# Kernel tuning notes

Measured on AMD Instinct MI355X. Metric: run time of the kernel, lower is better.

Reference implementation:

```python
import jax, jax.numpy as jnp
import numpy as np

# ---- static lookup-point config (matches cfg.radius/stride/level) ----
RADIUS = [4, 4, 4, 4]
STRIDE = [1, 1, 1, 1]
LEVEL = [0, 1, 2, 3]

def _build_pts():
    pts = {}
    for r, s, l in zip(RADIUS, STRIDE, LEVEL):
        pts.setdefault(l, set())
        for x in range(-r, r + 1):
            for y in range(-r, r + 1):
                pts[l].add((x * s, y * s))
    # sorted() reproduces torch's `v.sort()` on (x, y) tuples
    return {l: np.array(sorted(v), dtype=np.float32) for l, v in sorted(pts.items())}

PTS = _build_pts()                       # {lvl: (n_lvl, 2) offsets in level pixels}
N_LEVELS = max(LEVEL) + 1                # 4
CORR_DIM = 2 * sum(len(v) for v in PTS.values())   # 648
C_HALF = CORR_DIM // 2                   # 324 = per-direction channels
B, C, H, W = 1, 256, 80, 80


def _bilinear_sample(corr, x, y):
    """corr: (B, P, h, w); x, y: (P, n) pixel coords (align_corners=False convention,
    already converted to pixel space). Zero padding outside. Returns (B, P, n)."""
    Bn, P, h, w = corr.shape
    cf = corr.reshape(Bn, P, h * w)
    x0 = jnp.floor(x)
    y0 = jnp.floor(y)
    wx1 = x - x0
    wy1 = y - y0
    x0i = x0.astype(jnp.int32)
    y0i = y0.astype(jnp.int32)
    out = jnp.zeros((Bn, P, x.shape[-1]), corr.dtype)
    for dx, wxx in ((0, 1.0 - wx1), (1, wx1)):
        for dy, wyy in ((0, 1.0 - wy1), (1, wy1)):
            xi = x0i + dx
            yi = y0i + dy
            valid = (xi >= 0) & (xi < w) & (yi >= 0) & (yi < h)
            idx = jnp.clip(yi, 0, h - 1) * w + jnp.clip(xi, 0, w - 1)   # (P, n)
            v = jnp.take_along_axis(cf, jnp.broadcast_to(idx[None], (Bn,) + idx.shape), axis=2)
            out = out + v * (wxx * wyy * valid)[None]
    return out


def _lookup_pyramid(pyr):
    """pyr[lvl]: (B, P, H>>lvl, W>>lvl). Returns (B, P, C_HALF)."""
    outs = []
    for lvl, pts in PTS.items():
        s = 1 << lvl
        n = pts.shape[0]
        dxy = jnp.asarray(pts)
        # grid_sample align_corners=False: level-pixel coord of full-res pixel j is
        # (2j+1)/(2s) - 0.5; neighbor offsets are exactly `pts` in level pixels.
        bx = (2.0 * jnp.arange(W) + 1.0) / (2.0 * s) - 0.5   # (W,)
        by = (2.0 * jnp.arange(H) + 1.0) / (2.0 * s) - 0.5   # (H,)
        x = jnp.broadcast_to(bx[None, :, None] + dxy[None, None, :, 0], (H, W, n)).reshape(H * W, n)
        y = jnp.broadcast_to(by[:, None, None] + dxy[None, None, :, 1], (H, W, n)).reshape(H * W, n)
        outs.append(_bilinear_sample(pyr[lvl], x, y))
    return jnp.concatenate(outs, axis=-1)


def _pyramid(corr):
    """corr: (B, P, H, W) -> list of avg-pooled levels (2x2, stride 2)."""
    p = [corr]
    for _ in range(N_LEVELS - 1):
        b, pp, h, w = corr.shape
        corr = corr.reshape(b, pp, h // 2, 2, w // 2, 2).mean(axis=(3, 5))
        p.append(corr)
    return p


def _conv3x3_relu(x, w, b):
    y = jax.lax.conv_general_dilated(x, w, (1, 1), 'SAME',
                                     dimension_numbers=('NHWC', 'HWIO', 'NHWC'))
    return jax.nn.relu(y + b)


def _layer_norm(x, g, b, eps=1e-5):
    m = x.mean(-1, keepdims=True)
    v = ((x - m) ** 2).mean(-1, keepdims=True)
    return (x - m) * jax.lax.rsqrt(v + eps) * g + b


def setup_inputs() -> dict:
    key = jax.random.key(0)
    ks = jax.random.split(key, 4)
    return {
        'f0': jax.random.normal(ks[0], (B, C, H, W), jnp.float32),
        'f1': jax.random.normal(ks[1], (B, C, H, W), jnp.float32),
        'conv_w1': jax.random.normal(ks[2], (3, 3, C_HALF, C_HALF), jnp.float32) * 0.02,
        'conv_b1': jnp.zeros((C_HALF,), jnp.float32),
        'conv_w2': jax.random.normal(ks[3], (3, 3, C_HALF, C_HALF), jnp.float32) * 0.02,
        'conv_b2': jnp.zeros((C_HALF,), jnp.float32),
        'ln_g': jnp.ones((C_HALF,), jnp.float32),
        'ln_b': jnp.zeros((C_HALF,), jnp.float32),
    }


def reference(f0, f1, conv_w1, conv_b1, conv_w2, conv_b2, ln_g, ln_b):
    Bn, Cn, Hn, Wn = f0.shape
    P = Hn * Wn
    a = f0.reshape(Bn, Cn, P)
    bb = f1.reshape(Bn, Cn, P)
    corr01 = jnp.einsum('bcp,bcq->bpq', a, bb)          # (B, P, P)
    corr10 = jnp.swapaxes(corr01, 1, 2)
    feat01 = _lookup_pyramid(_pyramid(corr01.reshape(Bn, P, Hn, Wn)))   # (B, P, C_HALF)
    feat10 = _lookup_pyramid(_pyramid(corr10.reshape(Bn, P, Hn, Wn)))

    def branch(feat):
        x = feat.reshape(Bn, Hn, Wn, C_HALF)
        y = x + _conv3x3_relu(_conv3x3_relu(x, conv_w1, conv_b1), conv_w2, conv_b2)
        y = _layer_norm(y, ln_g, ln_b)
        return jnp.transpose(y, (0, 3, 1, 2))           # (B, C_HALF, H, W)

    return jnp.concatenate([branch(feat01), branch(feat10)], axis=1)    # (B, 2*C_HALF, H, W)
```

## Files before the change

kernel.cpp:

```cpp
#include <hip/hip_runtime.h>

typedef unsigned short u16;
typedef unsigned int   u32;
typedef float f32x4 __attribute__((ext_vector_type(4)));
typedef __bf16 bf16x8 __attribute__((ext_vector_type(8)));
typedef unsigned short u16x8 __attribute__((ext_vector_type(8)));

#define PP   6400
#define HH   80
#define WW   80
#define KC   256
#define CH   324
#define CPAD 384
#define PW   82
#define PPIX (PW*PW)
#define NPOOL 2176

__device__ inline float b2f(u16 u) { union { u32 i; float f; } v; v.i = ((u32)u) << 16; return v.f; }
__device__ inline u16 f2b(float f) {
    union { u32 i; float f; } v; v.f = f;
    u32 r = v.i + 0x7fffu + ((v.i >> 16) & 1u);
    return (u16)(r >> 16);
}

__device__ __forceinline__ void gload16(const void* g, void* l) {
    __builtin_amdgcn_global_load_lds((const __attribute__((address_space(1))) void*)g,
                                     (__attribute__((address_space(3))) void*)l, 16, 0, 0);
}

__global__ __launch_bounds__(256) void prep_f(const float* __restrict__ f0,
                                              const float* __restrict__ f1,
                                              u16* __restrict__ fA, u16* __restrict__ fB) {
    __shared__ float tile[64][65];
    int p0 = blockIdx.x * 64, c0 = blockIdx.y * 64;
    const float* src = blockIdx.z ? f1 : f0;
    u16* dst = blockIdx.z ? fB : fA;
    int tid = threadIdx.x;
#pragma unroll
    for (int it = 0; it < 16; ++it) {
        int idx = tid + it * 256;
        int cc = idx >> 6, pp = idx & 63;
        tile[cc][pp] = src[(size_t)(c0 + cc) * PP + p0 + pp];
    }
    __syncthreads();
#pragma unroll
    for (int it = 0; it < 16; ++it) {
        int idx = tid + it * 256;
        int pp = idx >> 6, cc = idx & 63;
        dst[(size_t)(p0 + pp) * KC + c0 + cc] = f2b(tile[cc][pp]);
    }
}

__global__ __launch_bounds__(256) void prep_w(const float* __restrict__ w1,
                                              const float* __restrict__ w2,
                                              u16* __restrict__ wT1, u16* __restrict__ wT2) {
    __shared__ float tile[64][65];
    int tap = blockIdx.x;
    int t6 = blockIdx.y;
    int ci0 = (t6 / 6) * 64, co0 = (t6 % 6) * 64;
    const float* w = blockIdx.z ? w2 : w1;
    u16* wT = blockIdx.z ? wT2 : wT1;
    int tid = threadIdx.x;
#pragma unroll
    for (int it = 0; it < 16; ++it) {
        int idx = tid + it * 256;
        int ciL = idx >> 6, coL = idx & 63;
        int ci = ci0 + ciL, co = co0 + coL;
        tile[ciL][coL] = (ci < CH && co < CH) ? w[((size_t)tap * CH + ci) * CH + co] : 0.f;
    }
    __syncthreads();
#pragma unroll
    for (int it = 0; it < 16; ++it) {
        int idx = tid + it * 256;
        int coL = idx >> 6, ciL = idx & 63;
        wT[((size_t)tap * CPAD + co0 + coL) * CPAD + ci0 + ciL] = f2b(tile[ciL][coL]);
    }
}

__global__ __launch_bounds__(384) void zero_border(u16* __restrict__ feat, u16* __restrict__ t1,
                                                   const float* __restrict__ b1,
                                                   const float* __restrict__ b2,
                                                   float* __restrict__ b1p, float* __restrict__ b2p) {
    int bi = blockIdx.x, dir = blockIdx.y;
    int t = threadIdx.x;
    if (bi == 324) {
        if (dir == 0) b1p[t] = t < CH ? b1[t] : 0.f;
        else          b2p[t] = t < CH ? b2[t] : 0.f;
        return;
    }
    int pix;
    if (bi < 82) pix = bi;
    else if (bi < 164) pix = 81 * PW + (bi - 82);
    else if (bi < 244) pix = (bi - 164 + 1) * PW;
    else pix = (bi - 244 + 1) * PW + 81;
    size_t off = ((size_t)dir * PPIX + pix) * CPAD + t;
    feat[off] = 0;
    t1[off] = 0;
}

__global__ __launch_bounds__(256) void pool_feat(const u16* __restrict__ fA,
                                                 const u16* __restrict__ fB,
                                                 u16* __restrict__ pbarA,
                                                 u16* __restrict__ pbarB) {
    int j = blockIdx.x;
    const u16* src = blockIdx.y ? fA : fB;
    u16* dst = blockIdx.y ? pbarA : pbarB;
    int k = threadIdx.x;
    int cy3 = j / 10, cx3 = j % 10;
    float l1v[16], l2v[4];
#pragma unroll
    for (int a = 0; a < 4; ++a)
#pragma unroll
        for (int b = 0; b < 4; ++b) {
            int cy = cy3 * 4 + a, cx = cx3 * 4 + b;
            int p00 = (2 * cy) * 80 + 2 * cx;
            float v = 0.25f * (b2f(src[(size_t)p00 * KC + k]) + b2f(src[(size_t)(p00 + 1) * KC + k]) +
                               b2f(src[(size_t)(p00 + 80) * KC + k]) + b2f(src[(size_t)(p00 + 81) * KC + k]));
            l1v[a * 4 + b] = v;
            dst[(size_t)(cy * 40 + cx) * KC + k] = f2b(v);
        }
#pragma unroll
    for (int a = 0; a < 2; ++a)
#pragma unroll
        for (int b = 0; b < 2; ++b) {
            float v = 0.25f * (l1v[(2 * a) * 4 + 2 * b] + l1v[(2 * a) * 4 + 2 * b + 1] +
                               l1v[(2 * a + 1) * 4 + 2 * b] + l1v[(2 * a + 1) * 4 + 2 * b + 1]);
            l2v[a * 2 + b] = v;
            dst[(size_t)(1600 + (cy3 * 2 + a) * 20 + cx3 * 2 + b) * KC + k] = f2b(v);
        }
    float v3 = 0.25f * (l2v[0] + l2v[1] + l2v[2] + l2v[3]);
    dst[(size_t)(2000 + j) * KC + k] = f2b(v3);
}

__global__ __launch_bounds__(256) void gemm_cp(const u16* __restrict__ fA,
                                               const u16* __restrict__ fB,
                                               const u16* __restrict__ pbarA,
                                               const u16* __restrict__ pbarB,
                                               u16* __restrict__ corr01,
                                               u16* __restrict__ corr10,
                                               u16* __restrict__ pc) {
    int y = blockIdx.y, z = blockIdx.z;
    bool band = (y < 7);
    int m0 = blockIdx.x * 128, n0;
    const u16 *Aptr, *Bptr;
    if (band) {
        if (z) return;
        int n0t = (int)blockIdx.x + y - 3;
        if (n0t < 0 || n0t >= 50) return;
        n0 = n0t * 128;
        Aptr = fA; Bptr = fB;
    } else {
        n0 = (y - 7) * 128;
        Aptr = z ? fB : fA;
        Bptr = z ? pbarA : pbarB;
    }
    __shared__ __align__(16) char smem[128 * 136 * 2];
    u16* As = (u16*)smem;
    u16* Bs = As + 128 * 64;
    u16* trans = (u16*)smem;
    const int TS = 136;
    int tid = threadIdx.x;
    int wave = tid >> 6, lane = tid & 63;
    int quad = lane >> 4, l16 = lane & 15;
    int lrow = lane >> 3, lchunk = lane & 7;
    int sc = lchunk ^ (lrow & 7);
    int sw = l16 & 7;
    int wr = (wave >> 1) * 64, wc = (wave & 1) * 64;
    f32x4 acc[4][4] = {};

    for (int k0 = 0; k0 < KC; k0 += 64) {
        __syncthreads();
#pragma unroll
        for (int i = 0; i < 4; ++i) {
            int row = i * 32 + wave * 8 + lrow;
            gload16(&Aptr[(size_t)(m0 + row) * KC + k0 + sc * 8], &As[(i * 32 + wave * 8) * 64]);
            gload16(&Bptr[(size_t)(n0 + row) * KC + k0 + sc * 8], &Bs[(i * 32 + wave * 8) * 64]);
        }
        __syncthreads();
#pragma unroll
        for (int ki = 0; ki < 2; ++ki) {
            bf16x8 af[4], bfr[4];
#pragma unroll
            for (int mi = 0; mi < 4; ++mi) {
                int r = wr + mi * 16 + l16;
                af[mi] = *(const bf16x8*)(&As[r * 64 + (((ki * 4 + quad) ^ sw) * 8)]);
            }
#pragma unroll
            for (int ni = 0; ni < 4; ++ni) {
                int r = wc + ni * 16 + l16;
                bfr[ni] = *(const bf16x8*)(&Bs[r * 64 + (((ki * 4 + quad) ^ sw) * 8)]);
            }
#pragma unroll
            for (int mi = 0; mi < 4; ++mi)
#pragma unroll
                for (int ni = 0; ni < 4; ++ni)
                    acc[mi][ni] = __builtin_amdgcn_mfma_f32_16x16x32_bf16(af[mi], bfr[ni], acc[mi][ni], 0, 0, 0);
        }
    }
    __syncthreads();
#pragma unroll
    for (int mi = 0; mi < 4; ++mi)
#pragma unroll
        for (int ni = 0; ni < 4; ++ni) {
            int rbase = wr + mi * 16 + quad * 4;
            int c = wc + ni * 16 + l16;
#pragma unroll
            for (int rr = 0; rr < 4; ++rr)
                trans[(rbase + rr) * TS + c] = f2b(acc[mi][ni][rr]);
        }
    __syncthreads();
    if (!band) {
        int dir = z;
#pragma unroll
        for (int it = 0; it < 8; ++it) {
            int r = it * 16 + (tid >> 4);
            int c8 = (tid & 15) * 8;
            u16x8 v = *(const u16x8*)(&trans[r * TS + c8]);
            *(u16x8*)(&pc[((size_t)dir * PP + m0 + r) * NPOOL + n0 + c8]) = v;
        }
        return;
    }
#pragma unroll
    for (int it = 0; it < 8; ++it) {
        int r = it * 16 + (tid >> 4);
        int c8 = (tid & 15) * 8;
        u16x8 v = *(const u16x8*)(&trans[r * TS + c8]);
        *(u16x8*)(&corr01[(size_t)(m0 + r) * PP + n0 + c8]) = v;
    }
    __syncthreads();
#pragma unroll
    for (int mi = 0; mi < 4; ++mi)
#pragma unroll
        for (int ni = 0; ni < 4; ++ni) {
            int c = wc + ni * 16 + l16;
            int rbase = wr + mi * 16 + quad * 4;
#pragma unroll
            for (int h = 0; h < 2; ++h) {
                u32 pk = (u32)f2b(acc[mi][ni][2 * h]) | ((u32)f2b(acc[mi][ni][2 * h + 1]) << 16);
                *(u32*)(&trans[c * TS + rbase + 2 * h]) = pk;
            }
        }
    __syncthreads();
#pragma unroll
    for (int it = 0; it < 8; ++it) {
        int c = it * 16 + (tid >> 4);
        int r8 = (tid & 15) * 8;
        u16x8 v = *(const u16x8*)(&trans[c * TS + r8]);
        *(u16x8*)(&corr10[(size_t)(n0 + c) * PP + m0 + r8]) = v;
    }
}

__global__ __launch_bounds__(384) void lookup(const u16* __restrict__ corr01,
                                              const u16* __restrict__ corr10,
                                              const u16* __restrict__ pc,
                                              u16* __restrict__ feat) {
    __shared__ __align__(16) u16 pcrow[4][NPOOL];
    __shared__ float l0buf[4][81];
    int p0 = blockIdx.x * 4, dir = blockIdx.y;
    int tid = threadIdx.x;
    const u16* corr = dir ? corr10 : corr01;
    for (int i = tid; i < 4 * (NPOOL / 8); i += 384) {
        int j = i / (NPOOL / 8), cc = i % (NPOOL / 8);
        *(u16x8*)(&pcrow[j][cc * 8]) =
            *(const u16x8*)(&pc[((size_t)dir * PP + p0 + j) * NPOOL + cc * 8]);
    }
    if (tid < 324) {
        int j = tid / 81, i = tid % 81;
        int p = p0 + j;
        int px = p % WW, py = p / WW;
        int dy = i / 9 - 4, dx = i % 9 - 4;
        int x = px + dx, yy = py + dy;
        float v = 0.f;
        if ((unsigned)x < (unsigned)WW && (unsigned)yy < (unsigned)HH)
            v = b2f(corr[(size_t)p * PP + yy * WW + x]);
        l0buf[j][(i % 9) * 9 + i / 9] = v;
    }
    __syncthreads();
    int ch = tid;
#pragma unroll
    for (int j = 0; j < 4; ++j) {
        int p = p0 + j;
        int px = p % WW, py = p / WW;
        float val = 0.f;
        if (ch < CH) {
            int lvl = ch / 81, i = ch % 81;
            if (lvl == 0) {
                val = l0buf[j][i];
            } else {
                int dx = i / 9 - 4, dy = i % 9 - 4;
                int wl = WW >> lvl;
                int base = (lvl == 1) ? 0 : (lvl == 2) ? 1600 : 2000;
                float inv = 1.0f / (float)(2 << lvl);
                float xc = (float)(2 * px + 1) * inv - 0.5f + (float)dx;
                float yc = (float)(2 * py + 1) * inv - 0.5f + (float)dy;
                float x0f = floorf(xc), y0f = floorf(yc);
                int x0 = (int)x0f, y0 = (int)y0f;
                float wx = xc - x0f, wy = yc - y0f;
#pragma unroll
                for (int cy = 0; cy < 2; ++cy)
#pragma unroll
                    for (int cx = 0; cx < 2; ++cx) {
                        int xi = x0 + cx, yi = y0 + cy;
                        if ((unsigned)xi < (unsigned)wl && (unsigned)yi < (unsigned)wl) {
                            float wgt = (cx ? wx : 1.f - wx) * (cy ? wy : 1.f - wy);
                            val += b2f(pcrow[j][base + yi * wl + xi]) * wgt;
                        }
                    }
            }
        }
        size_t pix = (size_t)(py + 1) * PW + px + 1;
        feat[((size_t)dir * PPIX + pix) * CPAD + ch] = f2b(val);
    }
}

__global__ __launch_bounds__(256) void conv_gemm(const u16* __restrict__ inFeat,
                                                 const u16* __restrict__ wTt,
                                                 const float* __restrict__ bias,
                                                 const u16* __restrict__ resid,
                                                 u16* __restrict__ outb) {
    int L = (int)blockIdx.x;
    int xcd = L & 7;
    int q = L >> 3;
    int n_t = q % 3; q /= 3;
    int mg = q % 13;
    int dir = q / 13;
    int m_t = mg * 8 + xcd;
    if (m_t >= 100) return;
    const u16* Ain = inFeat + (size_t)dir * PPIX * CPAD;
    const u16* Rin = resid ? resid + (size_t)dir * PPIX * CPAD : (const u16*)0;
    u16* Out = outb + (size_t)dir * PPIX * CPAD;
    __shared__ __align__(16) u16 As[64 * 128];
    __shared__ __align__(16) u16 Bs[128 * 128];
    int tid = threadIdx.x;
    int wave = tid >> 6, lane = tid & 63;
    int quad = lane >> 4, l16 = lane & 15;
    int wr = (wave >> 1) * 32, wc = (wave & 1) * 64;
    int m0 = m_t * 64, n0 = n_t * 128;
    f32x4 acc[2][4] = {};

    int pixA[4], scI[4];
#pragma unroll
    for (int i = 0; i < 4; ++i) {
        int r = wave * 16 + i * 4 + quad;
        int m = m0 + r;
        pixA[i] = (m / 80 + 1) * PW + (m % 80) + 1;
        scI[i] = l16 ^ ((i * 4 + quad) & 15);
    }

    for (int tap = 0; tap < 9; ++tap) {
        int dpix = (tap / 3 - 1) * PW + (tap % 3) - 1;
        const u16* Wt = wTt + ((size_t)tap * CPAD + n0) * CPAD;
#pragma unroll
        for (int kt = 0; kt < 3; ++kt) {
            int kc = kt * 128;
            __syncthreads();
#pragma unroll
            for (int i = 0; i < 4; ++i)
                gload16(&Ain[(size_t)(pixA[i] + dpix) * CPAD + kc + scI[i] * 8],
                        &As[(wave * 16 + i * 4) * 128]);
#pragma unroll
            for (int j = 0; j < 8; ++j) {
                int rb = wave * 32 + j * 4;
                gload16(&Wt[(size_t)(rb + quad) * CPAD + kc + scI[j & 3] * 8],
                        &Bs[rb * 128]);
            }
            __syncthreads();
#pragma unroll
            for (int ki = 0; ki < 4; ++ki) {
                int slot = (ki * 4 + quad) ^ l16;
                bf16x8 af[2], bfr[4];
#pragma unroll
                for (int mi = 0; mi < 2; ++mi)
                    af[mi] = *(const bf16x8*)(&As[(wr + mi * 16 + l16) * 128 + slot * 8]);
#pragma unroll
                for (int ni = 0; ni < 4; ++ni)
                    bfr[ni] = *(const bf16x8*)(&Bs[(wc + ni * 16 + l16) * 128 + slot * 8]);
#pragma unroll
                for (int mi = 0; mi < 2; ++mi)
#pragma unroll
                    for (int ni = 0; ni < 4; ++ni)
                        acc[mi][ni] = __builtin_amdgcn_mfma_f32_16x16x32_bf16(af[mi], bfr[ni], acc[mi][ni], 0, 0, 0);
            }
        }
    }
#pragma unroll
    for (int mi = 0; mi < 2; ++mi)
#pragma unroll
        for (int rr = 0; rr < 4; ++rr) {
            int p = m0 + wr + mi * 16 + quad * 4 + rr;
            size_t opix = (size_t)(p / 80 + 1) * PW + (p % 80) + 1;
#pragma unroll
            for (int ni = 0; ni < 4; ++ni) {
                int co = n0 + wc + ni * 16 + l16;
                float v = acc[mi][ni][rr] + bias[co];
                v = fmaxf(v, 0.f);
                if (Rin) v += b2f(Rin[opix * CPAD + co]);
                Out[opix * CPAD + co] = f2b(v);
            }
        }
}

__global__ __launch_bounds__(256) void ln_out(const u16* __restrict__ t2,
                                              const float* __restrict__ g,
                                              const float* __restrict__ b,
                                              float* __restrict__ out) {
    int dir = blockIdx.y;
    int p0 = blockIdx.x * 64;
    const u16* Y = t2 + (size_t)dir * PPIX * CPAD;
    __shared__ u16 buf[64 * 325];
    __shared__ float mean_s[64], inv_s[64];
    __shared__ float part[64][4][2];
    int tid = threadIdx.x;
    for (int idx = tid; idx < 64 * CH; idx += 256) {
        int pp = idx / CH, c = idx - pp * CH;
        int p = p0 + pp;
        size_t pix = (size_t)(p / 80 + 1) * PW + (p % 80) + 1;
        buf[pp * 325 + c] = Y[pix * CPAD + c];
    }
    __syncthreads();
    {
        int pp = tid >> 2, q = tid & 3;
        float s = 0.f, s2 = 0.f;
        for (int c = q; c < CH; c += 4) { float v = b2f(buf[pp * 325 + c]); s += v; s2 += v * v; }
        part[pp][q][0] = s; part[pp][q][1] = s2;
    }
    __syncthreads();
    if (tid < 64) {
        float s = 0.f, s2 = 0.f;
        for (int q = 0; q < 4; ++q) { s += part[tid][q][0]; s2 += part[tid][q][1]; }
        float m = s / (float)CH;
        float var = s2 / (float)CH - m * m;
        if (var < 0.f) var = 0.f;
        mean_s[tid] = m;
        inv_s[tid] = rsqrtf(var + 1e-5f);
    }
    __syncthreads();
    for (int idx = tid; idx < CH * 64; idx += 256) {
        int c = idx >> 6, pp = idx & 63;
        float v = (b2f(buf[pp * 325 + c]) - mean_s[pp]) * inv_s[pp] * g[c] + b[c];
        out[((size_t)(dir * CH + c)) * PP + p0 + pp] = v;
    }
}

extern "C" void kernel_launch(void* const* d_in, const int* in_sizes, int n_in,
                              void* d_out, int out_size, void* d_ws, size_t ws_size,
                              hipStream_t stream) {
    const float* f0  = (const float*)d_in[0];
    const float* f1  = (const float*)d_in[1];
    const float* w1  = (const float*)d_in[2];
    const float* b1  = (const float*)d_in[3];
    const float* w2  = (const float*)d_in[4];
    const float* b2  = (const float*)d_in[5];
    const float* lng = (const float*)d_in[6];
    const float* lnb = (const float*)d_in[7];
    float* out = (float*)d_out;

    char* ws = (char*)d_ws;
    size_t off = 0;
    auto alloc = [&](size_t bytes) -> char* {
        char* r = ws + off;
        off += (bytes + 511) & ~(size_t)511;
        return r;
    };
    u16* fA     = (u16*)alloc((size_t)PP * KC * 2);
    u16* fB     = (u16*)alloc((size_t)PP * KC * 2);
    u16* corr01 = (u16*)alloc((size_t)PP * PP * 2);
    u16* corr10 = (u16*)alloc((size_t)PP * PP * 2);
    u16* pc     = (u16*)alloc((size_t)2 * PP * NPOOL * 2);
    u16* feat   = (u16*)alloc((size_t)2 * PPIX * CPAD * 2);
    u16* t1     = (u16*)alloc((size_t)2 * PPIX * CPAD * 2);
    u16* t2     = (u16*)alloc((size_t)2 * PPIX * CPAD * 2);
    u16* pbarA  = (u16*)alloc((size_t)NPOOL * KC * 2);
    u16* pbarB  = (u16*)alloc((size_t)NPOOL * KC * 2);
    u16* wT1    = (u16*)alloc((size_t)9 * CPAD * CPAD * 2);
    u16* wT2    = (u16*)alloc((size_t)9 * CPAD * CPAD * 2);
    float* b1p  = (float*)alloc(CPAD * 4);
    float* b2p  = (float*)alloc(CPAD * 4);

    prep_f<<<dim3(100, 4, 2), 256, 0, stream>>>(f0, f1, fA, fB);
    prep_w<<<dim3(9, 36, 2), 256, 0, stream>>>(w1, w2, wT1, wT2);
    zero_border<<<dim3(325, 2), 384, 0, stream>>>(feat, t1, b1, b2, b1p, b2p);
    pool_feat<<<dim3(100, 2), 256, 0, stream>>>(fA, fB, pbarA, pbarB);
    gemm_cp<<<dim3(50, 24, 2), 256, 0, stream>>>(fA, fB, pbarA, pbarB, corr01, corr10, pc);
    lookup<<<dim3(1600, 2), 384, 0, stream>>>(corr01, corr10, pc, feat);
    conv_gemm<<<dim3(624), 256, 0, stream>>>(feat, wT1, b1p, (const u16*)0, t1);
    conv_gemm<<<dim3(624), 256, 0, stream>>>(t1, wT2, b2p, feat, t2);
    ln_out<<<dim3(100, 2), 256, 0, stream>>>(t2, lng, lnb, out);
}
```

Measured before the change: 259.7 us.

## Compute only the pooled-correlation window each row tile actually samples

Pooled correlation columns are now computed only for a window around each 128-row tile. That means 12 rows of level 1, 12 rows of level 2, and all of level 3, instead of all 2176 pooled columns. The pooled GEMM grid shrinks from 17 to 7 column tiles per direction, and the pc buffer and lookup shared memory shrink to 896 columns. The risk is correctness: the window must cover every bilinear tap for every pixel in the tile, and each lookup block must use the same window offsets as the GEMM.

After: 247.5 us. -4.7%, faster.

```diff
diff --git a/kernel.cpp b/kernel.cpp
--- a/kernel.cpp
+++ b/kernel.cpp
@@ -14,7 +14,7 @@
 #define CPAD 384
 #define PW   82
 #define PPIX (PW*PW)
-#define NPOOL 2176
+#define NP2  896
 
 __device__ inline float b2f(u16 u) { union { u32 i; float f; } v; v.i = ((u32)u) << 16; return v.f; }
 __device__ inline u16 f2b(float f) {
@@ -141,7 +141,7 @@
                                                u16* __restrict__ pc) {
     int y = blockIdx.y, z = blockIdx.z;
     bool band = (y < 7);
-    int m0 = blockIdx.x * 128, n0;
+    int m0 = blockIdx.x * 128, n0 = 0, jbase = 0;
     const u16 *Aptr, *Bptr;
     if (band) {
         if (z) return;
@@ -150,10 +150,14 @@
         n0 = n0t * 128;
         Aptr = fA; Bptr = fB;
     } else {
-        n0 = (y - 7) * 128;
+        jbase = (y - 7) * 128;
         Aptr = z ? fB : fA;
         Bptr = z ? pbarA : pbarB;
     }
+    int py0 = m0 / 80;
+    int s1 = min(max(py0 / 2 - 5, 0), 28);
+    int s2 = min(max(py0 / 4 - 5, 0), 8);
+
     __shared__ __align__(16) char smem[128 * 136 * 2];
     u16* As = (u16*)smem;
     u16* Bs = As + 128 * 64;
@@ -168,13 +172,28 @@
     int wr = (wave >> 1) * 64, wc = (wave & 1) * 64;
     f32x4 acc[4][4] = {};
 
+    size_t gRow[4];
+#pragma unroll
+    for (int i = 0; i < 4; ++i) {
+        int row = i * 32 + wave * 8 + lrow;
+        if (band) gRow[i] = (size_t)(n0 + row);
+        else {
+            int j = jbase + row;
+            int g = j < 480 ? s1 * 40 + j
+                  : j < 720 ? 1120 + s2 * 20 + j
+                  : j < 820 ? 1280 + j
+                  : 2099;
+            gRow[i] = (size_t)g;
+        }
+    }
+
     for (int k0 = 0; k0 < KC; k0 += 64) {
         __syncthreads();
 #pragma unroll
         for (int i = 0; i < 4; ++i) {
             int row = i * 32 + wave * 8 + lrow;
             gload16(&Aptr[(size_t)(m0 + row) * KC + k0 + sc * 8], &As[(i * 32 + wave * 8) * 64]);
-            gload16(&Bptr[(size_t)(n0 + row) * KC + k0 + sc * 8], &Bs[(i * 32 + wave * 8) * 64]);
+            gload16(&Bptr[gRow[i] * KC + k0 + sc * 8], &Bs[(i * 32 + wave * 8) * 64]);
         }
         __syncthreads();
 #pragma unroll
@@ -216,7 +235,7 @@
             int r = it * 16 + (tid >> 4);
             int c8 = (tid & 15) * 8;
             u16x8 v = *(const u16x8*)(&trans[r * TS + c8]);
-            *(u16x8*)(&pc[((size_t)dir * PP + m0 + r) * NPOOL + n0 + c8]) = v;
+            *(u16x8*)(&pc[((size_t)dir * PP + m0 + r) * NP2 + jbase + c8]) = v;
         }
         return;
     }
@@ -254,15 +273,19 @@
                                               const u16* __restrict__ corr10,
                                               const u16* __restrict__ pc,
                                               u16* __restrict__ feat) {
-    __shared__ __align__(16) u16 pcrow[4][NPOOL];
+    __shared__ __align__(16) u16 pcrow[4][NP2];
     __shared__ float l0buf[4][81];
     int p0 = blockIdx.x * 4, dir = blockIdx.y;
     int tid = threadIdx.x;
     const u16* corr = dir ? corr10 : corr01;
-    for (int i = tid; i < 4 * (NPOOL / 8); i += 384) {
-        int j = i / (NPOOL / 8), cc = i % (NPOOL / 8);
+    int mt = p0 >> 7;
+    int py0 = (mt * 128) / 80;
+    int s1 = min(max(py0 / 2 - 5, 0), 28);
+    int s2 = min(max(py0 / 4 - 5, 0), 8);
+    for (int i = tid; i < 4 * (NP2 / 8); i += 384) {
+        int j = i / (NP2 / 8), cc = i % (NP2 / 8);
         *(u16x8*)(&pcrow[j][cc * 8]) =
-            *(const u16x8*)(&pc[((size_t)dir * PP + p0 + j) * NPOOL + cc * 8]);
+            *(const u16x8*)(&pc[((size_t)dir * PP + p0 + j) * NP2 + cc * 8]);
     }
     if (tid < 324) {
         int j = tid / 81, i = tid % 81;
@@ -289,7 +312,6 @@
             } else {
                 int dx = i / 9 - 4, dy = i % 9 - 4;
                 int wl = WW >> lvl;
-                int base = (lvl == 1) ? 0 : (lvl == 2) ? 1600 : 2000;
                 float inv = 1.0f / (float)(2 << lvl);
                 float xc = (float)(2 * px + 1) * inv - 0.5f + (float)dx;
                 float yc = (float)(2 * py + 1) * inv - 0.5f + (float)dy;
@@ -303,7 +325,10 @@
                         int xi = x0 + cx, yi = y0 + cy;
                         if ((unsigned)xi < (unsigned)wl && (unsigned)yi < (unsigned)wl) {
                             float wgt = (cx ? wx : 1.f - wx) * (cy ? wy : 1.f - wy);
-                            val += b2f(pcrow[j][base + yi * wl + xi]) * wgt;
+                            int idx = (lvl == 1) ? (yi - s1) * 40 + xi
+                                    : (lvl == 2) ? 480 + (yi - s2) * 20 + xi
+                                                 : 720 + yi * 10 + xi;
+                            val += b2f(pcrow[j][idx]) * wgt;
                         }
                     }
             }
@@ -466,12 +491,12 @@
     u16* fB     = (u16*)alloc((size_t)PP * KC * 2);
     u16* corr01 = (u16*)alloc((size_t)PP * PP * 2);
     u16* corr10 = (u16*)alloc((size_t)PP * PP * 2);
-    u16* pc     = (u16*)alloc((size_t)2 * PP * NPOOL * 2);
+    u16* pc     = (u16*)alloc((size_t)2 * PP * NP2 * 2);
     u16* feat   = (u16*)alloc((size_t)2 * PPIX * CPAD * 2);
     u16* t1     = (u16*)alloc((size_t)2 * PPIX * CPAD * 2);
     u16* t2     = (u16*)alloc((size_t)2 * PPIX * CPAD * 2);
-    u16* pbarA  = (u16*)alloc((size_t)NPOOL * KC * 2);
-    u16* pbarB  = (u16*)alloc((size_t)NPOOL * KC * 2);
+    u16* pbarA  = (u16*)alloc((size_t)2176 * KC * 2);
+    u16* pbarB  = (u16*)alloc((size_t)2176 * KC * 2);
     u16* wT1    = (u16*)alloc((size_t)9 * CPAD * CPAD * 2);
     u16* wT2    = (u16*)alloc((size_t)9 * CPAD * CPAD * 2);
     float* b1p  = (float*)alloc(CPAD * 4);
@@ -481,7 +506,7 @@
     prep_w<<<dim3(9, 36, 2), 256, 0, stream>>>(w1, w2, wT1, wT2);
     zero_border<<<dim3(325, 2), 384, 0, stream>>>(feat, t1, b1, b2, b1p, b2p);
     pool_feat<<<dim3(100, 2), 256, 0, stream>>>(fA, fB, pbarA, pbarB);
-    gemm_cp<<<dim3(50, 24, 2), 256, 0, stream>>>(fA, fB, pbarA, pbarB, corr01, corr10, pc);
+    gemm_cp<<<dim3(50, 14, 2), 256, 0, stream>>>(fA, fB, pbarA, pbarB, corr01, corr10, pc);
     lookup<<<dim3(1600, 2), 384, 0, stream>>>(corr01, corr10, pc, feat);
     conv_gemm<<<dim3(624), 256, 0, stream>>>(feat, wT1, b1p, (const u16*)0, t1);
     conv_gemm<<<dim3(624), 256, 0, stream>>>(t1, wT2, b2p, feat, t2);
```
